# Performance work log

Hardware: AMD Instinct MI355X
Metric: run time of the kernel (lower is better)

Reference implementation:

```python
import jax, jax.numpy as jnp
import numpy as np

EPS = 0.5
MIN_SAMPLES = 5


def setup_inputs() -> dict:
    key = jax.random.key(0)
    X = jax.random.uniform(key, (12288, 8), dtype=jnp.float32)
    return {"X": X}


def reference(X):
    """DBSCAN: eps-range queries + cluster expansion, expressed as
    eps-graph connected components over core points (same clustering
    as the serial BFS in the original module; cluster ids are assigned
    in order of each cluster's minimum core index, matching the
    ascending-scan discovery order of the original)."""
    N = X.shape[0]
    SENTINEL = jnp.int32(N)

    # pairwise squared Euclidean distances [N, N] (KDTree range query equivalent)
    sq = jnp.sum(X * X, axis=1)
    d2 = sq[:, None] + sq[None, :] - 2.0 * (X @ X.T)
    adj = d2 <= (EPS * EPS)                      # eps-neighborhood (includes self)

    density = jnp.sum(adj, axis=1)               # |query_ball_point(x_i, eps)|
    core = density >= MIN_SAMPLES                # core-point mask

    # core-core edges: BFS expansion only propagates through cores
    core_adj = adj & core[None, :] & core[:, None]

    idx = jnp.arange(N, dtype=jnp.int32)
    init = jnp.where(core, idx, SENTINEL)        # each core starts as its own root

    def prop(lbl):
        # min label over core neighbors (min-plus propagation = connected components)
        nb_min = jnp.min(jnp.where(core_adj, lbl[None, :], SENTINEL), axis=1)
        return jnp.minimum(lbl, nb_min)

    def cond(state):
        cur, prev = state
        return jnp.any(cur != prev)

    def body(state):
        cur, _ = state
        return prop(cur), cur

    lbl, _ = jax.lax.while_loop(cond, body, (prop(init), init))

    # border points: non-core points within eps of a core join that core's cluster
    core_nb = jnp.min(jnp.where(adj & core[None, :], lbl[None, :], SENTINEL), axis=1)
    root = jnp.where(core, lbl, core_nb)         # SENTINEL -> noise

    # compact cluster ids: rank of each cluster root (min core index) ascending,
    # matching the original's sequential discovery order k = 0, 1, ...
    is_root = core & (lbl == idx)
    rank = jnp.cumsum(is_root.astype(jnp.int32)) - 1   # rank[i] valid where is_root[i]
    labels = jnp.where(root < SENTINEL,
                       rank[jnp.clip(root, 0, N - 1)],
                       jnp.int32(-1))
    return labels
```

## Files before the change

### kernel.cpp

```cpp
#include <hip/hip_runtime.h>

#define NPTS 12288
#define DIMS 8
#define EPS2 0.25f
#define MINS 5
#define NIB1 (NPTS / 256)
#define NW   (NPTS / 32)
#define SENT NPTS
#define RMAX 512
#define W    (RMAX / 32)
#define BIGL 0x3fffffff
#define FT   128
#define FB   256
#define FBGRID 256

#define ATHR 256
#define AROWS 2
#define ATI  (ATHR * AROWS)
#define ANIB (NPTS / ATI)
#define ANJB 48
#define AJC  (NPTS / ANJB)
#define AWCH (AJC / 32)

typedef float v2f __attribute__((ext_vector_type(2)));

__device__ __forceinline__ float dot8(const v2f* xi, const float4& a, const float4& b) {
  v2f y0 = {a.x, a.y}, y1 = {a.z, a.w}, y2 = {b.x, b.y}, y3 = {b.z, b.w};
  v2f d = xi[0] * y0;
  d = __builtin_elementwise_fma(xi[1], y1, d);
  d = __builtin_elementwise_fma(xi[2], y2, d);
  d = __builtin_elementwise_fma(xi[3], y3, d);
  return d.x + d.y;
}


__global__ __launch_bounds__(ATHR) void k_adj(const float* __restrict__ X,
                                              unsigned int* __restrict__ adj,
                                              int* __restrict__ density) {
  __shared__ float4 xs[AJC][2];
  __shared__ float sqs[AJC];
  int t = threadIdx.x;
  int j0 = blockIdx.y * AJC;
  {
    int j = j0 + t;
    float4 a = ((const float4*)X)[j * 2];
    float4 b = ((const float4*)X)[j * 2 + 1];
    xs[t][0] = a; xs[t][1] = b;
    float sv = 0.f;
    sv = fmaf(a.x, a.x, sv); sv = fmaf(a.y, a.y, sv); sv = fmaf(a.z, a.z, sv); sv = fmaf(a.w, a.w, sv);
    sv = fmaf(b.x, b.x, sv); sv = fmaf(b.y, b.y, sv); sv = fmaf(b.z, b.z, sv); sv = fmaf(b.w, b.w, sv);
    sqs[t] = sv;
  }
  int i0 = blockIdx.x * ATI + t, i1 = i0 + ATHR;
  v2f xi0[4], xi1[4];
  {
    float4 a0 = ((const float4*)X)[i0 * 2], b0v = ((const float4*)X)[i0 * 2 + 1];
    float4 a1 = ((const float4*)X)[i1 * 2], b1v = ((const float4*)X)[i1 * 2 + 1];
    xi0[0] = (v2f){a0.x, a0.y}; xi0[1] = (v2f){a0.z, a0.w};
    xi0[2] = (v2f){b0v.x, b0v.y}; xi0[3] = (v2f){b0v.z, b0v.w};
    xi1[0] = (v2f){a1.x, a1.y}; xi1[1] = (v2f){a1.z, a1.w};
    xi1[2] = (v2f){b1v.x, b1v.y}; xi1[3] = (v2f){b1v.z, b1v.w};
  }
  float sq0 = 0.f, sq1 = 0.f;
#pragma unroll
  for (int q = 0; q < 4; q++) {
    v2f p0 = xi0[q] * xi0[q], p1 = xi1[q] * xi1[q];
    sq0 += p0.x + p0.y; sq1 += p1.x + p1.y;
  }
  __syncthreads();
  unsigned int acc0[AWCH], acc1[AWCH];
#pragma unroll
  for (int w = 0; w < AWCH; w++) {
    unsigned int b0 = 0u, b1 = 0u;
#pragma unroll 4
    for (int bit = 0; bit < 32; bit++) {
      int jj = (w << 5) + bit;
      float4 xa = xs[jj][0], xb = xs[jj][1];
      float sj = sqs[jj];
      unsigned int m = 1u << bit;
      float d20 = (sq0 + sj) - 2.0f * dot8(xi0, xa, xb);
      float d21 = (sq1 + sj) - 2.0f * dot8(xi1, xa, xb);
      if (d20 <= EPS2) b0 |= m;
      if (d21 <= EPS2) b1 |= m;
    }
    acc0[w] = b0; acc1[w] = b1;
  }
  uint4* dst0 = (uint4*)(adj + (size_t)i0 * NW + blockIdx.y * AWCH);
  uint4* dst1 = (uint4*)(adj + (size_t)i1 * NW + blockIdx.y * AWCH);
  dst0[0] = make_uint4(acc0[0], acc0[1], acc0[2], acc0[3]);
  dst0[1] = make_uint4(acc0[4], acc0[5], acc0[6], acc0[7]);
  dst1[0] = make_uint4(acc1[0], acc1[1], acc1[2], acc1[3]);
  dst1[1] = make_uint4(acc1[4], acc1[5], acc1[6], acc1[7]);
  int pc0 = 0, pc1 = 0;
#pragma unroll
  for (int w = 0; w < AWCH; w++) { pc0 += __popc(acc0[w]); pc1 += __popc(acc1[w]); }
  atomicAdd(&density[i0], pc0);
  atomicAdd(&density[i1], pc1);
}

__global__ __launch_bounds__(256) void k_core(const int* __restrict__ density,
                                              unsigned long long* __restrict__ corebm,
                                              unsigned int* __restrict__ bm) {
  int t = threadIdx.x;
  if (blockIdx.x == 0) {
#pragma unroll
    for (int q = 0; q < RMAX * W / 256; q++) bm[t + q * 256] = 0u;
  }
  int i = blockIdx.x * 256 + t;
  unsigned long long m = __ballot(density[i] >= MINS);
  if ((t & 63) == 0) corebm[i >> 6] = m;
}

__global__ __launch_bounds__(256) void k_hookbm(const unsigned int* __restrict__ adj,
                                                const unsigned int* __restrict__ cb32,
                                                int* __restrict__ hook) {
  __shared__ unsigned int cb[NW];
  int t = threadIdx.x;
  for (int w = t; w < NW; w += 256) cb[w] = cb32[w];
  __syncthreads();
  int i = blockIdx.x * 256 + t;
  const unsigned int* row = adj + (size_t)i * NW;
  int wi = i >> 5;
  int m = i;
  for (int w = 0; w <= wi; w++) {
    unsigned int x = row[w] & cb[w];
    if (w == wi) x &= (1u << (i & 31)) - 1;
    if (x) { m = (w << 5) + __ffs(x) - 1; break; }
  }
  hook[i] = m;
}

__global__ __launch_bounds__(1024) void k_rid(const int* __restrict__ density,
                                              const int* __restrict__ hook,
                                              int* __restrict__ Rptr,
                                              int* __restrict__ labL,
                                              int* __restrict__ bcount) {
  __shared__ unsigned short ridS[NPTS];
  __shared__ int wsum[16];
  int t = threadIdx.x;
  int lane = t & 63, wid = t >> 6;
  const int SEG = NPTS / 1024;
  int base = t * SEG;
  int flags = 0;
  int s = 0;
#pragma unroll
  for (int k = 0; k < SEG; k++) {
    int i = base + k;
    int f = (density[i] >= MINS && hook[i] == i) ? 1 : 0;
    flags |= f << k;
    s += f;
  }
  int segsum = s;
#pragma unroll
  for (int off = 1; off < 64; off <<= 1) {
    int n = __shfl_up(s, off, 64);
    if (lane >= off) s += n;
  }
  if (lane == 63) wsum[wid] = s;
  __syncthreads();
  int woff = 0;
  for (int w = 0; w < wid; w++) woff += wsum[w];
  int run = woff + s - segsum;
#pragma unroll
  for (int k = 0; k < SEG; k++) {
    ridS[base + k] = (unsigned short)run;
    run += (flags >> k) & 1;
  }
  if (t == 1023) *Rptr = run;
  if (t == 0) *bcount = 0;
  __syncthreads();
  for (int k = 0; k < SEG; k++) {
    int i = base + k;
    int lab = -1;
    if (density[i] >= MINS) {
      int v = i, h = hook[v];
      while (h != v) { v = h; h = hook[v]; }
      lab = min((int)ridS[v], RMAX - 1);
    }
    labL[i] = lab;
  }
}

__global__ __launch_bounds__(FB) void k_fillbm(const unsigned int* __restrict__ adj,
                                               const unsigned int* __restrict__ cb32,
                                               const int* __restrict__ labL,
                                               unsigned int* __restrict__ bm) {
  __shared__ unsigned int bmL[RMAX * W];
  __shared__ unsigned short labS[NPTS];
  __shared__ unsigned int cb[NW];
  int t = threadIdx.x;
  for (int q = t; q < RMAX * W; q += FB) bmL[q] = 0u;
  for (int q = t; q < NPTS; q += FB) labS[q] = (unsigned short)(labL[q] + 1);
  for (int w = t; w < NW; w += FB) cb[w] = cb32[w];
  __syncthreads();
  int lane = t & 63, wv = t >> 6;
  int gw = blockIdx.x * 4 + wv;
  for (int i = gw; i < NPTS; i += 4 * FBGRID) {
    int a0 = (int)labS[i] - 1;
    if (a0 < 0) continue;
    const unsigned int* row = adj + (size_t)i * NW;
    int wi = i >> 5;
    for (int w = wi + lane; w < NW; w += 64) {
      unsigned int x = row[w] & cb[w];
      if (w == wi) x &= (0xFFFFFFFEu << (i & 31));
      while (x) {
        int b = __ffs(x) - 1; x &= x - 1;
        int lj = (int)labS[(w << 5) + b] - 1;
        if (lj != a0) {
          atomicOr(&bmL[a0 * W + (lj >> 5)], 1u << (lj & 31));
          atomicOr(&bmL[lj * W + (a0 >> 5)], 1u << (a0 & 31));
        }
      }
    }
  }
  __syncthreads();
  for (int q = t; q < RMAX * W; q += FB) {
    unsigned int v = bmL[q];
    if (v) atomicOr(&bm[q], v);
  }
}

__global__ __launch_bounds__(RMAX) void k_cc(const unsigned int* __restrict__ bm,
                                             const int* __restrict__ Rptr,
                                             int* __restrict__ clab) {
  __shared__ int lbl[RMAX];
  __shared__ int mn[RMAX];
  __shared__ int chg, cmp;
  int a = threadIdx.x;
  int R = *Rptr; if (R > RMAX) R = RMAX;
  lbl[a] = a;
  __syncthreads();
  while (true) {
    int m = lbl[a];
    if (a < R) {
      const unsigned int* row = bm + a * W;
#pragma unroll
      for (int w = 0; w < W; w++) {
        unsigned int bits = row[w];
        while (bits) {
          int b = __ffs(bits) - 1;
          bits &= bits - 1;
          m = min(m, lbl[(w << 5) + b]);
        }
      }
    }
    mn[a] = m;
    if (a == 0) chg = 0;
    __syncthreads();
    int l = lbl[a];
    if (m < l) { atomicMin(&lbl[l], m); atomicMin(&lbl[a], m); chg = 1; }
    __syncthreads();
    while (true) {
      if (a == 0) cmp = 0;
      __syncthreads();
      int nl = lbl[lbl[a]];
      __syncthreads();
      if (nl < lbl[a]) { lbl[a] = nl; cmp = 1; }
      __syncthreads();
      if (!cmp) break;
    }
    if (!chg) break;
    __syncthreads();
  }
  int flag = (a < R && lbl[a] == a) ? 1 : 0;
  mn[a] = flag;
  __syncthreads();
  for (int off = 1; off < RMAX; off <<= 1) {
    int v = mn[a];
    int add = (a >= off) ? mn[a - off] : 0;
    __syncthreads();
    mn[a] = v + add;
    __syncthreads();
  }
  clab[a] = mn[lbl[a]] - 1;
}

__global__ __launch_bounds__(256) void k_labels(const int* __restrict__ labL,
                                                const int* __restrict__ clab,
                                                int* __restrict__ labArr,
                                                int* __restrict__ blist,
                                                int* __restrict__ bcount,
                                                float* __restrict__ out) {
  int i = blockIdx.x * blockDim.x + threadIdx.x;
  if (i >= NPTS) return;
  int a = labL[i];
  if (a >= 0) {
    int lab = clab[a];
    labArr[i] = lab;
    out[i] = (float)lab;
  } else {
    labArr[i] = BIGL;
    out[i] = -1.0f;
    int pos = atomicAdd(bcount, 1);
    blist[pos] = i;
  }
}

__global__ __launch_bounds__(FT) void k_border(const unsigned int* __restrict__ adj,
                                               const unsigned int* __restrict__ cb32,
                                               const int* __restrict__ labArr,
                                               const int* __restrict__ blist,
                                               const int* __restrict__ bcount,
                                               float* __restrict__ out) {
  __shared__ unsigned int cb[NW];
  __shared__ int wm[FT / 64];
  int t = threadIdx.x;
  for (int w = t; w < NW; w += FT) cb[w] = cb32[w];
  __syncthreads();
  int count = *bcount;
  for (int k = blockIdx.x; k < count; k += gridDim.x) {
    int p = blist[k];
    const unsigned int* row = adj + (size_t)p * NW;
    int m = BIGL;
    for (int w = t; w < NW; w += FT) {
      unsigned int x = row[w] & cb[w];
      while (x) {
        int b = __ffs(x) - 1; x &= x - 1;
        m = min(m, labArr[(w << 5) + b]);
      }
    }
#pragma unroll
    for (int off = 32; off >= 1; off >>= 1) m = min(m, __shfl_xor(m, off, 64));
    if ((t & 63) == 0) wm[t >> 6] = m;
    __syncthreads();
    if (t == 0) {
      int mm = min(wm[0], wm[1]);
      out[p] = (mm < BIGL) ? (float)mm : -1.0f;
    }
    __syncthreads();
  }
}


extern "C" void kernel_launch(void* const* d_in, const int* in_sizes, int n_in,
                              void* d_out, int out_size, void* d_ws, size_t ws_size,
                              hipStream_t stream) {
  const float* X = (const float*)d_in[0];
  float* out = (float*)d_out;

  char* ws = (char*)d_ws;
  unsigned int* adj = (unsigned int*)ws;
  size_t off = (size_t)NPTS * NW * 4;
  int* density = (int*)(ws + off);           off += 4 * NPTS;
  int* hook    = (int*)(ws + off);           off += 4 * NPTS;
  int* labL    = (int*)(ws + off);           off += 4 * NPTS;
  int* labArr  = (int*)(ws + off);           off += 4 * NPTS;
  int* blist   = (int*)(ws + off);           off += 4 * NPTS;
  unsigned long long* corebm = (unsigned long long*)(ws + off); off += 2048;
  unsigned int* bm  = (unsigned int*)(ws + off); off += 4 * RMAX * W;
  int* clab    = (int*)(ws + off);           off += 4 * RMAX;
  int* Rptr    = (int*)(ws + off);
  int* bcount  = Rptr + 1;

  hipMemsetAsync(density, 0, 4 * NPTS, stream);

  dim3 gridA(ANIB, ANJB);

  k_adj<<<gridA, ATHR, 0, stream>>>(X, adj, density);
  k_core<<<NIB1, 256, 0, stream>>>(density, corebm, bm);
  k_hookbm<<<NIB1, 256, 0, stream>>>(adj, (const unsigned int*)corebm, hook);
  k_rid<<<1, 1024, 0, stream>>>(density, hook, Rptr, labL, bcount);
  k_fillbm<<<FBGRID, FB, 0, stream>>>(adj, (const unsigned int*)corebm, labL, bm);
  k_cc<<<1, RMAX, 0, stream>>>(bm, Rptr, clab);
  k_labels<<<NIB1, 256, 0, stream>>>(labL, clab, labArr, blist, bcount, out);
  k_border<<<256, FT, 0, stream>>>(adj, (const unsigned int*)corebm, labArr, blist, bcount, out);
}
```

Before: 228.2 us.

## Fuse core-mask into wave-parallel hook kernel and merge labeling into CC

Replaces the separate core-mask and hook kernels with one kernel in which every block recomputes the core bitmask into shared memory. One 64-lane wavefront then scans each adjacency row in parallel and takes the first core neighbour with a shuffle min-reduction, instead of one thread scanning serially. The label-writing kernel is folded into the single-block connected-components kernel, and the bitmap clearing moves to a memset. This removes two launches and the serial per-thread row scans. In exchange, each block repeats the density ballot, early exit from the row scan is lost, and the labelling pass now runs in a single block.

Result: slower. 241.5 us (+5.8%).

```diff
diff --git a/kernel.cpp b/kernel.cpp
--- a/kernel.cpp
+++ b/kernel.cpp
@@ -13,6 +13,8 @@
 #define FT   128
 #define FB   256
 #define FBGRID 256
+#define HB   96
+#define HT   512
 
 #define ATHR 256
 #define AROWS 2
@@ -98,36 +100,37 @@
   atomicAdd(&density[i1], pc1);
 }
 
-__global__ __launch_bounds__(256) void k_core(const int* __restrict__ density,
+__global__ __launch_bounds__(HT) void k_hook2(const unsigned int* __restrict__ adj,
+                                              const int* __restrict__ density,
                                               unsigned long long* __restrict__ corebm,
-                                              unsigned int* __restrict__ bm) {
-  int t = threadIdx.x;
+                                              int* __restrict__ hook) {
+  __shared__ unsigned long long cb64[NW / 2];
+  const unsigned int* cb = (const unsigned int*)cb64;
+  int t = threadIdx.x;
+  for (int base = 0; base < NPTS; base += HT) {
+    int i = base + t;
+    unsigned long long m = __ballot(density[i] >= MINS);
+    if ((t & 63) == 0) cb64[i >> 6] = m;
+  }
+  __syncthreads();
   if (blockIdx.x == 0) {
-#pragma unroll
-    for (int q = 0; q < RMAX * W / 256; q++) bm[t + q * 256] = 0u;
-  }
-  int i = blockIdx.x * 256 + t;
-  unsigned long long m = __ballot(density[i] >= MINS);
-  if ((t & 63) == 0) corebm[i >> 6] = m;
-}
-
-__global__ __launch_bounds__(256) void k_hookbm(const unsigned int* __restrict__ adj,
-                                                const unsigned int* __restrict__ cb32,
-                                                int* __restrict__ hook) {
-  __shared__ unsigned int cb[NW];
-  int t = threadIdx.x;
-  for (int w = t; w < NW; w += 256) cb[w] = cb32[w];
-  __syncthreads();
-  int i = blockIdx.x * 256 + t;
-  const unsigned int* row = adj + (size_t)i * NW;
-  int wi = i >> 5;
-  int m = i;
-  for (int w = 0; w <= wi; w++) {
-    unsigned int x = row[w] & cb[w];
-    if (w == wi) x &= (1u << (i & 31)) - 1;
-    if (x) { m = (w << 5) + __ffs(x) - 1; break; }
-  }
-  hook[i] = m;
+    for (int w = t; w < NW / 2; w += HT) corebm[w] = cb64[w];
+  }
+  int lane = t & 63, wv = t >> 6;
+  int gw = blockIdx.x * (HT / 64) + wv;
+  for (int i = gw; i < NPTS; i += (HT / 64) * HB) {
+    const unsigned int* row = adj + (size_t)i * NW;
+    int wi = i >> 5;
+    int m = i;
+    for (int w = lane; w <= wi; w += 64) {
+      unsigned int x = row[w] & cb[w];
+      if (w == wi) x &= (1u << (i & 31)) - 1;
+      if (x) m = min(m, (w << 5) + __ffs(x) - 1);
+    }
+#pragma unroll
+    for (int off = 32; off >= 1; off >>= 1) m = min(m, __shfl_xor(m, off, 64));
+    if (lane == 0) hook[i] = m;
+  }
 }
 
 __global__ __launch_bounds__(1024) void k_rid(const int* __restrict__ density,
@@ -222,7 +225,11 @@
 
 __global__ __launch_bounds__(RMAX) void k_cc(const unsigned int* __restrict__ bm,
                                              const int* __restrict__ Rptr,
-                                             int* __restrict__ clab) {
+                                             const int* __restrict__ labL,
+                                             int* __restrict__ labArr,
+                                             int* __restrict__ blist,
+                                             int* __restrict__ bcount,
+                                             float* __restrict__ out) {
   __shared__ int lbl[RMAX];
   __shared__ int mn[RMAX];
   __shared__ int chg, cmp;
@@ -272,27 +279,22 @@
     mn[a] = v + add;
     __syncthreads();
   }
-  clab[a] = mn[lbl[a]] - 1;
-}
-
-__global__ __launch_bounds__(256) void k_labels(const int* __restrict__ labL,
-                                                const int* __restrict__ clab,
-                                                int* __restrict__ labArr,
-                                                int* __restrict__ blist,
-                                                int* __restrict__ bcount,
-                                                float* __restrict__ out) {
-  int i = blockIdx.x * blockDim.x + threadIdx.x;
-  if (i >= NPTS) return;
-  int a = labL[i];
-  if (a >= 0) {
-    int lab = clab[a];
-    labArr[i] = lab;
-    out[i] = (float)lab;
-  } else {
-    labArr[i] = BIGL;
-    out[i] = -1.0f;
-    int pos = atomicAdd(bcount, 1);
-    blist[pos] = i;
+  int myclab = mn[lbl[a]] - 1;
+  mn[a] = myclab;
+  __syncthreads();
+  for (int base = 0; base < NPTS; base += RMAX) {
+    int i = base + a;
+    int l = labL[i];
+    if (l >= 0) {
+      int lab = mn[l];
+      labArr[i] = lab;
+      out[i] = (float)lab;
+    } else {
+      labArr[i] = BIGL;
+      out[i] = -1.0f;
+      int pos = atomicAdd(bcount, 1);
+      blist[pos] = i;
+    }
   }
 }
 
@@ -348,20 +350,18 @@
   int* blist   = (int*)(ws + off);           off += 4 * NPTS;
   unsigned long long* corebm = (unsigned long long*)(ws + off); off += 2048;
   unsigned int* bm  = (unsigned int*)(ws + off); off += 4 * RMAX * W;
-  int* clab    = (int*)(ws + off);           off += 4 * RMAX;
   int* Rptr    = (int*)(ws + off);
   int* bcount  = Rptr + 1;
 
   hipMemsetAsync(density, 0, 4 * NPTS, stream);
+  hipMemsetAsync(bm, 0, 4 * RMAX * W, stream);
 
   dim3 gridA(ANIB, ANJB);
 
   k_adj<<<gridA, ATHR, 0, stream>>>(X, adj, density);
-  k_core<<<NIB1, 256, 0, stream>>>(density, corebm, bm);
-  k_hookbm<<<NIB1, 256, 0, stream>>>(adj, (const unsigned int*)corebm, hook);
+  k_hook2<<<HB, HT, 0, stream>>>(adj, density, corebm, hook);
   k_rid<<<1, 1024, 0, stream>>>(density, hook, Rptr, labL, bcount);
   k_fillbm<<<FBGRID, FB, 0, stream>>>(adj, (const unsigned int*)corebm, labL, bm);
-  k_cc<<<1, RMAX, 0, stream>>>(bm, Rptr, clab);
-  k_labels<<<NIB1, 256, 0, stream>>>(labL, clab, labArr, blist, bcount, out);
+  k_cc<<<1, RMAX, 0, stream>>>(bm, Rptr, labL, labArr, blist, bcount, out);
   k_border<<<256, FT, 0, stream>>>(adj, (const unsigned int*)corebm, labArr, blist, bcount, out);
 }
```

## Build adjacency bitmask with wave ballots and compute density in separate popcount pass

Applied to the files above, without the earlier changes.

The adjacency kernel now evaluates one j point per iteration across a wave of i points and packs the results with a 64-bit ballot. Lane 0 writes the words for row j, which relies on the matrix being symmetric, instead of each thread accumulating per-row bit words in registers. This removes per-thread bit packing, register arrays and per-thread atomics. Density moves to a new kernel that popcounts each adjacency row with a wave reduction, which replaces the memset and atomicAdds. The cost is many small 8-byte stores from a single lane per ballot and an extra pass over the 18 MB bitmask.

Result: slower. 275.8 us (+20.9%).

```diff
diff --git a/kernel.cpp b/kernel.cpp
--- a/kernel.cpp
+++ b/kernel.cpp
@@ -6,7 +6,6 @@
 #define MINS 5
 #define NIB1 (NPTS / 256)
 #define NW   (NPTS / 32)
-#define SENT NPTS
 #define RMAX 512
 #define W    (RMAX / 32)
 #define BIGL 0x3fffffff
@@ -15,12 +14,10 @@
 #define FBGRID 256
 
 #define ATHR 256
-#define AROWS 2
-#define ATI  (ATHR * AROWS)
-#define ANIB (NPTS / ATI)
-#define ANJB 48
-#define AJC  (NPTS / ANJB)
-#define AWCH (AJC / 32)
+#define AI   512
+#define ANIB (NPTS / AI)
+#define AJC  256
+#define ANJB (NPTS / AJC)
 
 typedef float v2f __attribute__((ext_vector_type(2)));
 
@@ -33,69 +30,76 @@
   return d.x + d.y;
 }
 
+__device__ __forceinline__ float sq8(const float4& a, const float4& b) {
+  float s = 0.f;
+  s = fmaf(a.x, a.x, s); s = fmaf(a.y, a.y, s); s = fmaf(a.z, a.z, s); s = fmaf(a.w, a.w, s);
+  s = fmaf(b.x, b.x, s); s = fmaf(b.y, b.y, s); s = fmaf(b.z, b.z, s); s = fmaf(b.w, b.w, s);
+  return s;
+}
+
 
 __global__ __launch_bounds__(ATHR) void k_adj(const float* __restrict__ X,
-                                              unsigned int* __restrict__ adj,
-                                              int* __restrict__ density) {
+                                              unsigned int* __restrict__ adj) {
   __shared__ float4 xs[AJC][2];
   __shared__ float sqs[AJC];
   int t = threadIdx.x;
+  int lane = t & 63, wv = t >> 6;
   int j0 = blockIdx.y * AJC;
   {
     int j = j0 + t;
     float4 a = ((const float4*)X)[j * 2];
     float4 b = ((const float4*)X)[j * 2 + 1];
     xs[t][0] = a; xs[t][1] = b;
-    float sv = 0.f;
-    sv = fmaf(a.x, a.x, sv); sv = fmaf(a.y, a.y, sv); sv = fmaf(a.z, a.z, sv); sv = fmaf(a.w, a.w, sv);
-    sv = fmaf(b.x, b.x, sv); sv = fmaf(b.y, b.y, sv); sv = fmaf(b.z, b.z, sv); sv = fmaf(b.w, b.w, sv);
-    sqs[t] = sv;
-  }
-  int i0 = blockIdx.x * ATI + t, i1 = i0 + ATHR;
+    sqs[t] = sq8(a, b);
+  }
+  int ib = blockIdx.x * AI;
+  int i0 = ib + wv * 64 + lane, i1 = i0 + 256;
   v2f xi0[4], xi1[4];
+  float sq0, sq1;
   {
-    float4 a0 = ((const float4*)X)[i0 * 2], b0v = ((const float4*)X)[i0 * 2 + 1];
-    float4 a1 = ((const float4*)X)[i1 * 2], b1v = ((const float4*)X)[i1 * 2 + 1];
+    float4 a0 = ((const float4*)X)[i0 * 2], b0 = ((const float4*)X)[i0 * 2 + 1];
+    float4 a1 = ((const float4*)X)[i1 * 2], b1 = ((const float4*)X)[i1 * 2 + 1];
     xi0[0] = (v2f){a0.x, a0.y}; xi0[1] = (v2f){a0.z, a0.w};
-    xi0[2] = (v2f){b0v.x, b0v.y}; xi0[3] = (v2f){b0v.z, b0v.w};
+    xi0[2] = (v2f){b0.x, b0.y}; xi0[3] = (v2f){b0.z, b0.w};
     xi1[0] = (v2f){a1.x, a1.y}; xi1[1] = (v2f){a1.z, a1.w};
-    xi1[2] = (v2f){b1v.x, b1v.y}; xi1[3] = (v2f){b1v.z, b1v.w};
-  }
-  float sq0 = 0.f, sq1 = 0.f;
-#pragma unroll
-  for (int q = 0; q < 4; q++) {
-    v2f p0 = xi0[q] * xi0[q], p1 = xi1[q] * xi1[q];
-    sq0 += p0.x + p0.y; sq1 += p1.x + p1.y;
-  }
-  __syncthreads();
-  unsigned int acc0[AWCH], acc1[AWCH];
-#pragma unroll
-  for (int w = 0; w < AWCH; w++) {
-    unsigned int b0 = 0u, b1 = 0u;
+    xi1[2] = (v2f){b1.x, b1.y}; xi1[3] = (v2f){b1.z, b1.w};
+    sq0 = sq8(a0, b0);
+    sq1 = sq8(a1, b1);
+  }
+  __syncthreads();
 #pragma unroll 4
-    for (int bit = 0; bit < 32; bit++) {
-      int jj = (w << 5) + bit;
-      float4 xa = xs[jj][0], xb = xs[jj][1];
-      float sj = sqs[jj];
-      unsigned int m = 1u << bit;
-      float d20 = (sq0 + sj) - 2.0f * dot8(xi0, xa, xb);
-      float d21 = (sq1 + sj) - 2.0f * dot8(xi1, xa, xb);
-      if (d20 <= EPS2) b0 |= m;
-      if (d21 <= EPS2) b1 |= m;
-    }
-    acc0[w] = b0; acc1[w] = b1;
-  }
-  uint4* dst0 = (uint4*)(adj + (size_t)i0 * NW + blockIdx.y * AWCH);
-  uint4* dst1 = (uint4*)(adj + (size_t)i1 * NW + blockIdx.y * AWCH);
-  dst0[0] = make_uint4(acc0[0], acc0[1], acc0[2], acc0[3]);
-  dst0[1] = make_uint4(acc0[4], acc0[5], acc0[6], acc0[7]);
-  dst1[0] = make_uint4(acc1[0], acc1[1], acc1[2], acc1[3]);
-  dst1[1] = make_uint4(acc1[4], acc1[5], acc1[6], acc1[7]);
-  int pc0 = 0, pc1 = 0;
-#pragma unroll
-  for (int w = 0; w < AWCH; w++) { pc0 += __popc(acc0[w]); pc1 += __popc(acc1[w]); }
-  atomicAdd(&density[i0], pc0);
-  atomicAdd(&density[i1], pc1);
+  for (int jj = 0; jj < AJC; jj++) {
+    float4 xa = xs[jj][0], xb = xs[jj][1];
+    float sj = sqs[jj];
+    float d20 = (sq0 + sj) - 2.0f * dot8(xi0, xa, xb);
+    float d21 = (sq1 + sj) - 2.0f * dot8(xi1, xa, xb);
+    unsigned long long b0 = __ballot(d20 <= EPS2);
+    unsigned long long b1 = __ballot(d21 <= EPS2);
+    unsigned long long* rowq =
+        (unsigned long long*)(adj + (size_t)(j0 + jj) * NW) + (ib >> 6);
+    if (lane == 0) {
+      rowq[wv] = b0;
+      rowq[wv + 4] = b1;
+    }
+  }
+}
+
+__global__ __launch_bounds__(256) void k_dens(const unsigned int* __restrict__ adj,
+                                              int* __restrict__ density) {
+  int t = threadIdx.x, lane = t & 63, wv = t >> 6;
+  int gw = blockIdx.x * 4 + wv;
+  for (int i = gw; i < NPTS; i += 384) {
+    const uint4* row = (const uint4*)(adj + (size_t)i * NW);
+    uint4 v = row[lane];
+    int s = __popc(v.x) + __popc(v.y) + __popc(v.z) + __popc(v.w);
+    if (lane < 32) {
+      uint4 v2 = row[64 + lane];
+      s += __popc(v2.x) + __popc(v2.y) + __popc(v2.z) + __popc(v2.w);
+    }
+#pragma unroll
+    for (int off = 32; off >= 1; off >>= 1) s += __shfl_xor(s, off, 64);
+    if (lane == 0) density[i] = s;
+  }
 }
 
 __global__ __launch_bounds__(256) void k_core(const int* __restrict__ density,
@@ -347,16 +351,15 @@
   int* labArr  = (int*)(ws + off);           off += 4 * NPTS;
   int* blist   = (int*)(ws + off);           off += 4 * NPTS;
   unsigned long long* corebm = (unsigned long long*)(ws + off); off += 2048;
-  unsigned int* bm  = (unsigned int*)(ws + off); off += 4 * RMAX * W;
+  unsigned int* bm = (unsigned int*)(ws + off); off += 4 * RMAX * W;
   int* clab    = (int*)(ws + off);           off += 4 * RMAX;
   int* Rptr    = (int*)(ws + off);
   int* bcount  = Rptr + 1;
 
-  hipMemsetAsync(density, 0, 4 * NPTS, stream);
-
   dim3 gridA(ANIB, ANJB);
 
-  k_adj<<<gridA, ATHR, 0, stream>>>(X, adj, density);
+  k_adj<<<gridA, ATHR, 0, stream>>>(X, adj);
+  k_dens<<<96, 256, 0, stream>>>(adj, density);
   k_core<<<NIB1, 256, 0, stream>>>(density, corebm, bm);
   k_hookbm<<<NIB1, 256, 0, stream>>>(adj, (const unsigned int*)corebm, hook);
   k_rid<<<1, 1024, 0, stream>>>(density, hook, Rptr, labL, bcount);
```
